# Kernel tuning notes

Measured on AMD Instinct MI355X. Metric: run time of the kernel, lower is better.

The kernel has to match this reference:

```python
import jax, jax.numpy as jnp
import numpy as np

B, N, C = 4, 16384, 512
HEADS = 16
HEADC = C // HEADS
HIDDEN = int(C * 4.0)


def setup_inputs() -> dict:
    key = jax.random.key(0)
    ks = jax.random.split(key, 8)
    s1 = 1.0 / np.sqrt(C)
    s2 = 1.0 / np.sqrt(HIDDEN)
    return {
        "x": jax.random.normal(ks[0], (B, N, C), jnp.float32),
        "mask_matrix": jnp.zeros((1,), jnp.int32),
        "norm1_w": jnp.ones((C,), jnp.float32),
        "norm1_b": jnp.zeros((C,), jnp.float32),
        "kln_w": jnp.ones((HEADS, 1, HEADC), jnp.float32),
        "kln_b": jnp.zeros((HEADS, 1, HEADC), jnp.float32),
        "vln_w": jnp.ones((HEADS, 1, HEADC), jnp.float32),
        "vln_b": jnp.zeros((HEADS, 1, HEADC), jnp.float32),
        "norm2_w": jnp.ones((C,), jnp.float32),
        "norm2_b": jnp.zeros((C,), jnp.float32),
        "fc1_w": jax.random.uniform(ks[1], (HIDDEN, C), jnp.float32, -s1, s1),
        "fc1_b": jax.random.uniform(ks[2], (HIDDEN,), jnp.float32, -s1, s1),
        "fc2_w": jax.random.uniform(ks[3], (C, HIDDEN), jnp.float32, -s2, s2),
        "fc2_b": jax.random.uniform(ks[4], (C,), jnp.float32, -s2, s2),
    }


def _ln(t, w, b, eps=1e-5):
    # standard nn.LayerNorm: biased variance, eps inside sqrt
    mean = t.mean(-1, keepdims=True)
    var = ((t - mean) ** 2).mean(-1, keepdims=True)
    return w * (t - mean) / jnp.sqrt(var + eps) + b


def _ln_std(t, w, b, eps=1e-5):
    # custom LayerNorm: unbiased std (torch.std), eps added to std
    d = t.shape[-1]
    mean = t.mean(-1, keepdims=True)
    var = ((t - mean) ** 2).sum(-1, keepdims=True) / (d - 1)
    return w * ((t - mean) / (jnp.sqrt(var) + eps)) + b


def reference(x, mask_matrix, norm1_w, norm1_b, kln_w, kln_b, vln_w, vln_b,
              norm2_w, norm2_b, fc1_w, fc1_b, fc2_w, fc2_b):
    b, n, c = x.shape
    shortcut = x
    h = _ln(x, norm1_w, norm1_b)
    # simple_attn (softmax-free linear attention)
    qkv = h.reshape(b, n, HEADS, HEADC).transpose(0, 2, 1, 3)  # [B,H,N,D]
    q = qkv
    k = _ln_std(qkv, kln_w, kln_b)
    v = _ln_std(qkv, vln_w, vln_b)
    kv = jnp.einsum('bhnd,bhne->bhde', k, v) / n        # [B,H,D,D]
    attn = jnp.einsum('bhnd,bhde->bhne', q, kv)          # [B,H,N,D]
    attn = attn.transpose(0, 2, 1, 3).reshape(b, n, c)
    h = attn + h                                          # residual inside simple_attn (bias = x post-norm1)
    x = shortcut + h
    # MLP branch
    m = _ln(x, norm2_w, norm2_b)
    m = jax.nn.gelu(m @ fc1_w.T + fc1_b, approximate=False)
    m = m @ fc2_w.T + fc2_b
    return x + m
```

## Files before the change

kernel.cpp:

```cpp
#include <hip/hip_runtime.h>
#include <cstdint>

#define BB 4
#define NN 16384
#define CC 512
#define HH 16
#define DD 32
#define HID 2048
#define MTOT (BB * NN)

typedef __bf16 bf16_t;
typedef __bf16 bf16x8 __attribute__((ext_vector_type(8)));
typedef __bf16 bf16x4 __attribute__((ext_vector_type(4)));
typedef float  f32x4  __attribute__((ext_vector_type(4)));
typedef float  f32x16 __attribute__((ext_vector_type(16)));

__device__ __forceinline__ void gload_lds16(const void* g, void* l) {
  auto gp = reinterpret_cast<const __attribute__((address_space(1))) char*>(
      reinterpret_cast<uintptr_t>(g));
  auto lp = reinterpret_cast<__attribute__((address_space(3))) char*>(
      reinterpret_cast<uintptr_t>(l));
  __builtin_amdgcn_global_load_lds(gp, lp, 16, 0, 0);
}

__global__ __launch_bounds__(256) void cvt_bf16_kernel(const float* __restrict__ src,
                                                       bf16_t* __restrict__ dst) {
  const long i = ((long)blockIdx.x * 256 + threadIdx.x) * 4;
  const f32x4 v = *(const f32x4*)(src + i);
  bf16x4 o;
  o[0] = (bf16_t)v[0]; o[1] = (bf16_t)v[1]; o[2] = (bf16_t)v[2]; o[3] = (bf16_t)v[3];
  *(bf16x4*)(dst + i) = o;
}

__global__ __launch_bounds__(256) void norm1_kernel(const float* __restrict__ x,
                                                    const float* __restrict__ w,
                                                    const float* __restrict__ bvec,
                                                    bf16_t* __restrict__ h) {
  const int wv = threadIdx.x >> 6, l = threadIdx.x & 63;
  const long tok = (long)blockIdx.x * 4 + wv;
  const int c0 = l * 8;
  const f32x4 a = *(const f32x4*)(x + tok * CC + c0);
  const f32x4 b = *(const f32x4*)(x + tok * CC + c0 + 4);
  float v[8];
#pragma unroll
  for (int i = 0; i < 4; ++i) { v[i] = a[i]; v[4 + i] = b[i]; }
  float s = 0.f, s2 = 0.f;
#pragma unroll
  for (int i = 0; i < 8; ++i) { s += v[i]; s2 += v[i] * v[i]; }
  for (int off = 32; off; off >>= 1) { s += __shfl_xor(s, off); s2 += __shfl_xor(s2, off); }
  const float mean = s * (1.f / CC);
  const float var  = fmaxf(s2 * (1.f / CC) - mean * mean, 0.f);
  const float rstd = rsqrtf(var + 1e-5f);
  const f32x4 w0 = *(const f32x4*)(w + c0), w1 = *(const f32x4*)(w + c0 + 4);
  const f32x4 b0 = *(const f32x4*)(bvec + c0), b1 = *(const f32x4*)(bvec + c0 + 4);
  bf16x8 o;
#pragma unroll
  for (int i = 0; i < 4; ++i) {
    o[i]     = (bf16_t)(w0[i] * (v[i] - mean) * rstd + b0[i]);
    o[4 + i] = (bf16_t)(w1[i] * (v[4 + i] - mean) * rstd + b1[i]);
  }
  *(bf16x8*)(h + tok * CC + c0) = o;
}

__global__ __launch_bounds__(256) void kv_partial_kernel(const bf16_t* __restrict__ h,
                                                         const float* __restrict__ klw,
                                                         const float* __restrict__ klb,
                                                         const float* __restrict__ vlw,
                                                         const float* __restrict__ vlb,
                                                         float* __restrict__ kvp) {
  __shared__ bf16_t kb[256 * 32];
  __shared__ bf16_t vb[256 * 32];
  __shared__ float scratch[192 * 16];
  const int tid = threadIdx.x;
  const int bh = blockIdx.x >> 6, chunk = blockIdx.x & 63;
  const int head = bh & 15;
  const int b = bh >> 4;
  const long tok0 = ((long)b << 14) + chunk * 256;
  const bf16_t* src = h + (tok0 + tid) * (long)CC + head * DD;
  float hv[32];
  {
    float s = 0.f, s2 = 0.f;
#pragma unroll
    for (int c = 0; c < 4; ++c) {
      const bf16x8 r = *(const bf16x8*)(src + c * 8);
#pragma unroll
      for (int j = 0; j < 8; ++j) {
        hv[c * 8 + j] = (float)r[j]; s += hv[c * 8 + j]; s2 += hv[c * 8 + j] * hv[c * 8 + j];
      }
    }
    const float mean = s * (1.f / 32.f);
    const float varu = fmaxf((s2 - 32.f * mean * mean) * (1.f / 31.f), 0.f);
    const float inv = 1.f / (sqrtf(varu) + 1e-5f);
    const int sx = (tid >> 1) & 3;
#pragma unroll
    for (int c = 0; c < 4; ++c) {
      bf16x8 kc, vc;
#pragma unroll
      for (int j = 0; j < 8; ++j) {
        const int d = c * 8 + j;
        const float t = (hv[d] - mean) * inv;
        kc[j] = (bf16_t)(klw[head * DD + d] * t + klb[head * DD + d]);
        vc[j] = (bf16_t)(vlw[head * DD + d] * t + vlb[head * DD + d]);
      }
      *(bf16x8*)((char*)kb + tid * 64 + ((c ^ sx) * 16)) = kc;
      *(bf16x8*)((char*)vb + tid * 64 + ((c ^ sx) * 16)) = vc;
    }
  }
  __syncthreads();
  const int g = tid >> 6, l = tid & 63;
  const int d0 = (l >> 3) * 4, e0 = (l & 7) * 4;
  const int ck = (l >> 3) >> 1, hk = (l >> 3) & 1;
  const int ce = (l & 7) >> 1, he = l & 1;
  float a[4][4] = {};
  for (int t = g; t < 256; t += 4) {
    const int tx = (t >> 1) & 3;
    const bf16x4 kq = *(const bf16x4*)((const char*)kb + t * 64 + ((ck ^ tx) * 16) + hk * 8);
    const bf16x4 vq = *(const bf16x4*)((const char*)vb + t * 64 + ((ce ^ tx) * 16) + he * 8);
    float kf[4], vf[4];
#pragma unroll
    for (int i2 = 0; i2 < 4; ++i2) { kf[i2] = (float)kq[i2]; vf[i2] = (float)vq[i2]; }
#pragma unroll
    for (int i2 = 0; i2 < 4; ++i2)
#pragma unroll
      for (int j2 = 0; j2 < 4; ++j2) a[i2][j2] += kf[i2] * vf[j2];
  }
  __syncthreads();
  if (g) {
#pragma unroll
    for (int i2 = 0; i2 < 4; ++i2)
#pragma unroll
      for (int j2 = 0; j2 < 4; ++j2)
        scratch[((g - 1) * 64 + l) * 16 + i2 * 4 + j2] = a[i2][j2];
  }
  __syncthreads();
  if (!g) {
#pragma unroll
    for (int gg = 0; gg < 3; ++gg)
#pragma unroll
      for (int i2 = 0; i2 < 4; ++i2)
#pragma unroll
        for (int j2 = 0; j2 < 4; ++j2)
          a[i2][j2] += scratch[(gg * 64 + l) * 16 + i2 * 4 + j2];
    float* dst = kvp + ((long)(bh * 64 + chunk) << 10);
#pragma unroll
    for (int i2 = 0; i2 < 4; ++i2) {
      f32x4 st;
      st[0] = a[i2][0]; st[1] = a[i2][1]; st[2] = a[i2][2]; st[3] = a[i2][3];
      *(f32x4*)&dst[(d0 + i2) * 32 + e0] = st;
    }
  }
}

__global__ __launch_bounds__(256) void kv_reduce_kernel(const float* __restrict__ kvp,
                                                        bf16_t* __restrict__ kvT) {
  const int bh = blockIdx.x;
  const int i4 = threadIdx.x * 4;
  const int d = i4 >> 5, e0 = i4 & 31;
  float s[4] = {};
  const float* p = kvp + ((long)bh << 16) + i4;
  for (int ch = 0; ch < 64; ++ch) {
    const f32x4 t = *(const f32x4*)(p + (ch << 10));
    s[0] += t[0]; s[1] += t[1]; s[2] += t[2]; s[3] += t[3];
  }
  const float sc = 1.f / (float)NN;
  bf16_t* q = kvT + ((long)bh << 10);
#pragma unroll
  for (int j = 0; j < 4; ++j) q[(e0 + j) * 32 + d] = (bf16_t)(s[j] * sc);
}

#define ASTRIDE 520
__global__ __launch_bounds__(256) void attn_fused_kernel(const float* __restrict__ x,
                                                         const bf16_t* __restrict__ h,
                                                         const bf16_t* __restrict__ kvTg,
                                                         const float* __restrict__ n2w,
                                                         const float* __restrict__ n2b,
                                                         float* __restrict__ xout,
                                                         bf16_t* __restrict__ mout) {
  __shared__ bf16_t attn_s[32 * ASTRIDE];
  const int tid = threadIdx.x;
  const int wv = tid >> 6, lane = tid & 63;
  const int lr = lane & 15, kg = lane >> 4;
  const long tok0 = (long)blockIdx.x * 32;
  const int b = (int)(tok0 >> 14);
  const bf16_t* kvsrc = kvTg + ((long)b << 14);

  {
    const int tt = wv & 1, hh = wv >> 1;
    const bf16_t* arow = h + (tok0 + tt * 16 + lr) * (long)CC + kg * 8;
    const f32x4 zero = {};
#pragma unroll
    for (int hi = 0; hi < 8; ++hi) {
      const int hd = hh * 8 + hi;
      const bf16_t* kvh = kvsrc + (hd << 10) + kg * 8;
      const bf16x8 af = *(const bf16x8*)(arow + hd * DD);
      const bf16x8 b0 = *(const bf16x8*)(kvh + lr * 32);
      const bf16x8 b1 = *(const bf16x8*)(kvh + (16 + lr) * 32);
      const f32x4 a0 = __builtin_amdgcn_mfma_f32_16x16x32_bf16(af, b0, zero, 0, 0, 0);
      const f32x4 a1 = __builtin_amdgcn_mfma_f32_16x16x32_bf16(af, b1, zero, 0, 0, 0);
      const int rbase = tt * 16 + kg * 4;
#pragma unroll
      for (int rg = 0; rg < 4; ++rg) {
        attn_s[(rbase + rg) * ASTRIDE + hd * 32 + lr]      = (bf16_t)a0[rg];
        attn_s[(rbase + rg) * ASTRIDE + hd * 32 + 16 + lr] = (bf16_t)a1[rg];
      }
    }
  }

  const int c0 = lane * 8;
  const f32x4 w0 = *(const f32x4*)(n2w + c0), w1 = *(const f32x4*)(n2w + c0 + 4);
  const f32x4 bb0 = *(const f32x4*)(n2b + c0), bb1 = *(const f32x4*)(n2b + c0 + 4);

  const long tokp = tok0 + wv * 8;
  f32x4 xa = *(const f32x4*)(x + tokp * CC + c0);
  f32x4 xb = *(const f32x4*)(x + tokp * CC + c0 + 4);
  bf16x8 hv = *(const bf16x8*)(h + tokp * CC + c0);
  __syncthreads();

#pragma unroll
  for (int it = 0; it < 8; ++it) {
    const int tl = wv * 8 + it;
    const long tok = tok0 + tl;
    f32x4 xa1, xb1;
    bf16x8 hv1;
    if (it < 7) {
      xa1 = *(const f32x4*)(x + (tok + 1) * CC + c0);
      xb1 = *(const f32x4*)(x + (tok + 1) * CC + c0 + 4);
      hv1 = *(const bf16x8*)(h + (tok + 1) * CC + c0);
    }
    const bf16x8 av = *(const bf16x8*)&attn_s[tl * ASTRIDE + c0];
    float x2[8];
#pragma unroll
    for (int i = 0; i < 4; ++i) {
      x2[i]     = xa[i] + (float)hv[i]     + (float)av[i];
      x2[4 + i] = xb[i] + (float)hv[4 + i] + (float)av[4 + i];
    }
    float s = 0.f, s2 = 0.f;
#pragma unroll
    for (int i = 0; i < 8; ++i) { s += x2[i]; s2 += x2[i] * x2[i]; }
    for (int off = 32; off; off >>= 1) { s += __shfl_xor(s, off); s2 += __shfl_xor(s2, off); }
    const float mean = s * (1.f / CC);
    const float var  = fmaxf(s2 * (1.f / CC) - mean * mean, 0.f);
    const float rstd = rsqrtf(var + 1e-5f);
    f32x4 oa, ob;
    bf16x8 om;
#pragma unroll
    for (int i = 0; i < 4; ++i) {
      oa[i] = x2[i]; ob[i] = x2[4 + i];
      om[i]     = (bf16_t)(w0[i] * (x2[i] - mean) * rstd + bb0[i]);
      om[4 + i] = (bf16_t)(w1[i] * (x2[4 + i] - mean) * rstd + bb1[i]);
    }
    *(f32x4*)(xout + tok * CC + c0) = oa;
    *(f32x4*)(xout + tok * CC + c0 + 4) = ob;
    *(bf16x8*)(mout + tok * CC + c0) = om;
    xa = xa1; xb = xb1; hv = hv1;
  }
}

template <int K, int NOUT, int BN, bool GELU>
__global__ __launch_bounds__(512, 2) void gemm8p_kernel(const bf16_t* __restrict__ A,
                                                        const bf16_t* __restrict__ Bw,
                                                        const float* __restrict__ bias,
                                                        bf16_t* __restrict__ outb,
                                                        float* __restrict__ outf) {
  constexpr int NTILE = NOUT / BN;
  constexpr int NT = K / 64;
  constexpr int NI = NT / 2;
  constexpr int WNSPAN = BN / 4;
  constexpr int NF2 = WNSPAN / 32;
  constexpr int BLOADS = BN / 128;
  constexpr int ABYT = 32768;
  constexpr int BBYT = BN * 128;
  constexpr int BUFB = ABYT + BBYT;
  constexpr int KSB = BN * 64;

  __shared__ char lds[2 * BUFB];

  const int tid = threadIdx.x;
  const int wid = tid >> 6, lane = tid & 63;
  const int wm = wid >> 2, wn = wid & 3;
  const int l31 = lane & 31, kg5 = lane >> 5;

  int bid = blockIdx.x;
  const int qq = gridDim.x >> 3;
  bid = (bid & 7) * qq + (bid >> 3);
  const long row0 = (long)(bid / NTILE) * 256;
  const long col0 = (long)(bid % NTILE) * BN;

  const int srow = tid >> 2;
  const int sce = (((tid & 3) ^ ((srow >> 1) & 3)) << 3);
  const bf16_t* pA = A + (row0 + srow) * (long)K + sce;
  const bf16_t* pB = Bw + (col0 + srow) * (long)K + sce;
  char* ldsp = (char*)lds;

  auto SA = [&](int buf, int ks, int kt) {
    char* d_ = ldsp + buf * BUFB + ks * 16384 + tid * 16;
    const bf16_t* g_ = pA + (long)kt * 64 + ks * 32;
    gload_lds16(g_, d_);
    gload_lds16(g_ + 128L * K, d_ + 8192);
  };
  auto SB = [&](int buf, int ks, int kt) {
    char* d_ = ldsp + buf * BUFB + ABYT + ks * KSB + tid * 16;
    const bf16_t* g_ = pB + (long)kt * 64 + ks * 32;
    gload_lds16(g_, d_);
    if constexpr (BLOADS == 2) gload_lds16(g_ + 128L * K, d_ + 8192);
  };

  f32x16 acc[4][NF2] = {};
  bf16x8 af[4], bf[NF2];

  const int swz = (l31 >> 1) & 3;
  const int cb0 = (((0 << 1) | kg5) ^ swz) << 4;
  const int cb1 = (((1 << 1) | kg5) ^ swz) << 4;
  const char* aR = ldsp + (wm * 128 + l31) * 64;
  const char* bR = ldsp + ABYT + (wn * WNSPAN + l31) * 64;

  auto RD = [&](int buf, int ks, int k16) {
    const int cb = k16 ? cb1 : cb0;
    const char* a_ = aR + buf * BUFB + ks * 16384 + cb;
    const char* b_ = bR + buf * BUFB + ks * KSB + cb;
#pragma unroll
    for (int mf = 0; mf < 4; ++mf) af[mf] = *(const bf16x8*)(a_ + mf * 2048);
#pragma unroll
    for (int nf = 0; nf < NF2; ++nf) bf[nf] = *(const bf16x8*)(b_ + nf * 2048);
  };
  auto MM = [&]() {
    __builtin_amdgcn_s_setprio(1);
#pragma unroll
    for (int mf = 0; mf < 4; ++mf)
#pragma unroll
      for (int nf = 0; nf < NF2; ++nf)
        acc[mf][nf] =
            __builtin_amdgcn_mfma_f32_32x32x16_bf16(af[mf], bf[nf], acc[mf][nf], 0, 0, 0);
    __builtin_amdgcn_s_setprio(0);
  };
  auto W2U = [&]() {
    if constexpr (BLOADS == 2) asm volatile("s_waitcnt vmcnt(8)" ::: "memory");
    else                       asm volatile("s_waitcnt vmcnt(6)" ::: "memory");
  };
  auto W1U = [&]() {
    if constexpr (BLOADS == 2) asm volatile("s_waitcnt vmcnt(4)" ::: "memory");
    else                       asm volatile("s_waitcnt vmcnt(3)" ::: "memory");
  };
#define BARX() __builtin_amdgcn_s_barrier()
#define LGKM0() asm volatile("s_waitcnt lgkmcnt(0)" ::: "memory")
#define W0U() asm volatile("s_waitcnt vmcnt(0)" ::: "memory")

  SA(0, 0, 0); SB(0, 0, 0);
  SA(0, 1, 0); SB(0, 1, 0);
  SA(1, 0, 1); SB(1, 0, 1);
  W2U();
  BARX();

  for (int i = 0; i < NI; ++i) {
    const int t1 = 2 * i + 1, tA = 2 * i + 2, tB = 2 * i + 3;
    RD(0, 0, 0); SA(1, 1, t1);
    BARX(); LGKM0(); MM(); BARX();
    RD(0, 0, 1); SB(1, 1, t1);
    BARX(); LGKM0(); MM(); W2U(); BARX();
    RD(0, 1, 0); if (tA < NT) SA(0, 0, tA);
    BARX(); LGKM0(); MM(); BARX();
    RD(0, 1, 1); if (tA < NT) SB(0, 0, tA);
    BARX(); LGKM0(); MM();
    if (tA < NT) W2U(); else W1U();
    BARX();
    RD(1, 0, 0); if (tA < NT) SA(0, 1, tA);
    BARX(); LGKM0(); MM(); BARX();
    RD(1, 0, 1); if (tA < NT) SB(0, 1, tA);
    BARX(); LGKM0(); MM();
    if (tA < NT) W2U(); else W0U();
    BARX();
    RD(1, 1, 0); if (tB < NT) SA(1, 0, tB);
    BARX(); LGKM0(); MM(); BARX();
    RD(1, 1, 1); if (tB < NT) SB(1, 0, tB);
    BARX(); LGKM0(); MM();
    if (tB < NT) W2U();
    BARX();
  }
#undef BARX
#undef LGKM0
#undef W0U

#pragma unroll
  for (int mf = 0; mf < 4; ++mf) {
#pragma unroll
    for (int nf = 0; nf < NF2; ++nf) {
      const long col = col0 + wn * WNSPAN + nf * 32 + l31;
      const float bs = bias[col];
#pragma unroll
      for (int r = 0; r < 16; ++r) {
        const long row = row0 + wm * 128 + mf * 32 + (r & 3) + 8 * (r >> 2) + 4 * kg5;
        const float v = acc[mf][nf][r] + bs;
        if constexpr (GELU) {
          const float u = 0.7978845608028654f * (v + 0.044715f * v * v * v);
          const float gv = v / (1.f + __expf(-2.f * u));
          outb[row * NOUT + col] = (bf16_t)gv;
        } else {
          outf[row * NOUT + col] += v;
        }
      }
    }
  }
}

extern "C" void kernel_launch(void* const* d_in, const int* in_sizes, int n_in,
                              void* d_out, int out_size, void* d_ws, size_t ws_size,
                              hipStream_t stream) {
  const float* x   = (const float*)d_in[0];
  const float* n1w = (const float*)d_in[2];
  const float* n1b = (const float*)d_in[3];
  const float* klw = (const float*)d_in[4];
  const float* klb = (const float*)d_in[5];
  const float* vlw = (const float*)d_in[6];
  const float* vlb = (const float*)d_in[7];
  const float* n2w = (const float*)d_in[8];
  const float* n2b = (const float*)d_in[9];
  const float* w1f = (const float*)d_in[10];
  const float* b1  = (const float*)d_in[11];
  const float* w2f = (const float*)d_in[12];
  const float* b2  = (const float*)d_in[13];
  float* out = (float*)d_out;

  int nch;
  if (ws_size >= 423755776ULL)      nch = 1;
  else if (ws_size >= 289538048ULL) nch = 2;
  else                              nch = 4;
  const long mch = MTOT / nch;

  char* ws = (char*)d_ws;
  size_t off = 0;
  bf16_t* h   = (bf16_t*)(ws + off); off += (size_t)MTOT * CC * 2;
  bf16_t* mb  = (bf16_t*)(ws + off); off += (size_t)MTOT * CC * 2;
  bf16_t* act = (bf16_t*)(ws + off); off += (size_t)mch * HID * 2;
  bf16_t* w1  = (bf16_t*)(ws + off); off += (size_t)HID * CC * 2;
  bf16_t* w2  = (bf16_t*)(ws + off); off += (size_t)HID * CC * 2;
  float*  kvp = (float*)(ws + off);  off += (size_t)BB * HH * 64 * 1024 * 4;
  bf16_t* kvT = (bf16_t*)(ws + off);

  cvt_bf16_kernel<<<1024, 256, 0, stream>>>(w1f, w1);
  cvt_bf16_kernel<<<1024, 256, 0, stream>>>(w2f, w2);
  norm1_kernel<<<MTOT / 4, 256, 0, stream>>>(x, n1w, n1b, h);
  kv_partial_kernel<<<BB * HH * 64, 256, 0, stream>>>(h, klw, klb, vlw, vlb, kvp);
  kv_reduce_kernel<<<BB * HH, 256, 0, stream>>>(kvp, kvT);
  attn_fused_kernel<<<MTOT / 32, 256, 0, stream>>>(x, h, kvT, n2w, n2b, out, mb);
  for (int ch = 0; ch < nch; ++ch) {
    gemm8p_kernel<CC, HID, 256, true>
        <<<(int)((mch / 256) * (HID / 256)), 512, 0, stream>>>(
        mb + (size_t)ch * mch * CC, w1, b1, act, nullptr);
    if (mch >= 32768) {
      gemm8p_kernel<HID, CC, 256, false>
          <<<(int)((mch / 256) * (CC / 256)), 512, 0, stream>>>(
          act, w2, b2, nullptr, out + (size_t)ch * mch * CC);
    } else {
      gemm8p_kernel<HID, CC, 128, false>
          <<<(int)((mch / 256) * (CC / 128)), 512, 0, stream>>>(
          act, w2, b2, nullptr, out + (size_t)ch * mch * CC);
    }
  }
}
```

Baseline: 589.0 us.

## Store residual in bf16 scratch, write output once, and change LDS swizzle

The attention kernel now writes the post-attention residual x2 as bf16 into a new workspace buffer instead of fp32 into the output. The fc2 GEMM epilogue then writes out = x2b + v directly, replacing a read-modify-write of fp32 output. This halves the residual write and drops the fp32 output read in the epilogue, at the cost of rounding the residual to bf16. The LDS XOR swizzle gains an extra term to reduce bank conflicts, and the chunk-count thresholds change (nch=1 is removed) because the extra buffer uses more workspace.

```diff
diff --git a/kernel.cpp b/kernel.cpp
--- a/kernel.cpp
+++ b/kernel.cpp
@@ -174,7 +174,7 @@
                                                          const bf16_t* __restrict__ kvTg,
                                                          const float* __restrict__ n2w,
                                                          const float* __restrict__ n2b,
-                                                         float* __restrict__ xout,
+                                                         bf16_t* __restrict__ x2b,
                                                          bf16_t* __restrict__ mout) {
   __shared__ bf16_t attn_s[32 * ASTRIDE];
   const int tid = threadIdx.x;
@@ -241,16 +241,15 @@
     const float mean = s * (1.f / CC);
     const float var  = fmaxf(s2 * (1.f / CC) - mean * mean, 0.f);
     const float rstd = rsqrtf(var + 1e-5f);
-    f32x4 oa, ob;
-    bf16x8 om;
+    bf16x8 ox, om;
 #pragma unroll
     for (int i = 0; i < 4; ++i) {
-      oa[i] = x2[i]; ob[i] = x2[4 + i];
+      ox[i]     = (bf16_t)x2[i];
+      ox[4 + i] = (bf16_t)x2[4 + i];
       om[i]     = (bf16_t)(w0[i] * (x2[i] - mean) * rstd + bb0[i]);
       om[4 + i] = (bf16_t)(w1[i] * (x2[4 + i] - mean) * rstd + bb1[i]);
     }
-    *(f32x4*)(xout + tok * CC + c0) = oa;
-    *(f32x4*)(xout + tok * CC + c0 + 4) = ob;
+    *(bf16x8*)(x2b + tok * CC + c0) = ox;
     *(bf16x8*)(mout + tok * CC + c0) = om;
     xa = xa1; xb = xb1; hv = hv1;
   }
@@ -261,7 +260,8 @@
                                                         const bf16_t* __restrict__ Bw,
                                                         const float* __restrict__ bias,
                                                         bf16_t* __restrict__ outb,
-                                                        float* __restrict__ outf) {
+                                                        float* __restrict__ outf,
+                                                        const bf16_t* __restrict__ x2b) {
   constexpr int NTILE = NOUT / BN;
   constexpr int NT = K / 64;
   constexpr int NI = NT / 2;
@@ -287,7 +287,8 @@
   const long col0 = (long)(bid % NTILE) * BN;
 
   const int srow = tid >> 2;
-  const int sce = (((tid & 3) ^ ((srow >> 1) & 3)) << 3);
+  const int ssw = (((srow >> 1) & 3) ^ ((srow >> 3) & 3));
+  const int sce = (((tid & 3) ^ ssw) << 3);
   const bf16_t* pA = A + (row0 + srow) * (long)K + sce;
   const bf16_t* pB = Bw + (col0 + srow) * (long)K + sce;
   char* ldsp = (char*)lds;
@@ -308,7 +309,7 @@
   f32x16 acc[4][NF2] = {};
   bf16x8 af[4], bf[NF2];
 
-  const int swz = (l31 >> 1) & 3;
+  const int swz = ((l31 >> 1) & 3) ^ ((l31 >> 3) & 3);
   const int cb0 = (((0 << 1) | kg5) ^ swz) << 4;
   const int cb1 = (((1 << 1) | kg5) ^ swz) << 4;
   const char* aR = ldsp + (wm * 128 + l31) * 64;
@@ -395,7 +396,7 @@
           const float gv = v / (1.f + __expf(-2.f * u));
           outb[row * NOUT + col] = (bf16_t)gv;
         } else {
-          outf[row * NOUT + col] += v;
+          outf[row * NOUT + col] = (float)x2b[row * NOUT + col] + v;
         }
       }
     }
@@ -421,15 +422,15 @@
   float* out = (float*)d_out;
 
   int nch;
-  if (ws_size >= 423755776ULL)      nch = 1;
-  else if (ws_size >= 289538048ULL) nch = 2;
-  else                              nch = 4;
+  if (ws_size >= 360000000ULL) nch = 2;
+  else                         nch = 4;
   const long mch = MTOT / nch;
 
   char* ws = (char*)d_ws;
   size_t off = 0;
   bf16_t* h   = (bf16_t*)(ws + off); off += (size_t)MTOT * CC * 2;
   bf16_t* mb  = (bf16_t*)(ws + off); off += (size_t)MTOT * CC * 2;
+  bf16_t* x2b = (bf16_t*)(ws + off); off += (size_t)MTOT * CC * 2;
   bf16_t* act = (bf16_t*)(ws + off); off += (size_t)mch * HID * 2;
   bf16_t* w1  = (bf16_t*)(ws + off); off += (size_t)HID * CC * 2;
   bf16_t* w2  = (bf16_t*)(ws + off); off += (size_t)HID * CC * 2;
@@ -441,19 +442,21 @@
   norm1_kernel<<<MTOT / 4, 256, 0, stream>>>(x, n1w, n1b, h);
   kv_partial_kernel<<<BB * HH * 64, 256, 0, stream>>>(h, klw, klb, vlw, vlb, kvp);
   kv_reduce_kernel<<<BB * HH, 256, 0, stream>>>(kvp, kvT);
-  attn_fused_kernel<<<MTOT / 32, 256, 0, stream>>>(x, h, kvT, n2w, n2b, out, mb);
+  attn_fused_kernel<<<MTOT / 32, 256, 0, stream>>>(x, h, kvT, n2w, n2b, x2b, mb);
   for (int ch = 0; ch < nch; ++ch) {
     gemm8p_kernel<CC, HID, 256, true>
         <<<(int)((mch / 256) * (HID / 256)), 512, 0, stream>>>(
-        mb + (size_t)ch * mch * CC, w1, b1, act, nullptr);
+        mb + (size_t)ch * mch * CC, w1, b1, act, nullptr, nullptr);
     if (mch >= 32768) {
       gemm8p_kernel<HID, CC, 256, false>
           <<<(int)((mch / 256) * (CC / 256)), 512, 0, stream>>>(
-          act, w2, b2, nullptr, out + (size_t)ch * mch * CC);
+          act, w2, b2, nullptr, out + (size_t)ch * mch * CC,
+          x2b + (size_t)ch * mch * CC);
     } else {
       gemm8p_kernel<HID, CC, 128, false>
           <<<(int)((mch / 256) * (CC / 128)), 512, 0, stream>>>(
-          act, w2, b2, nullptr, out + (size_t)ch * mch * CC);
-    }
-  }
-}
+          act, w2, b2, nullptr, out + (size_t)ch * mch * CC,
+          x2b + (size_t)ch * mch * CC);
+    }
+  }
+}
```

Result: faster. 573.4 us, median of 4 (-2.7%).
